# Optimization experiments

Measured on AMD Instinct MI355X. Metric: run time of the kernel, lower is better.

Reference implementation:

```python
import jax, jax.numpy as jnp
import numpy as np

HN, ND, STRIDE, ESTRIDE = 10, 40, 3, 3  # hidden_node, ndim, stride, encode_stride


def _build_graphs():
    # Dense aggregation matrices A[dst, src] equivalent to the module's fixed
    # edge lists (scatter-add of src features into dst). Graph is tiny (10/40
    # nodes) and identical across the batch, so dense matmul is the efficient
    # exact form of the gather->scatter-add.
    w = np.float32(np.exp(-(1.0 / STRIDE) ** 2))
    A_pred = np.zeros((HN, HN), np.float32)
    for j in range(HN):
        A_pred[j, j] += 1.0                      # edge [j, j], weight 1
        for dj in range(1, STRIDE - 1):          # dj = 1 only
            A_pred[(j - dj) % HN, j] += w        # edge [j, j-dj]
            A_pred[(j + dj) % HN, j] += w        # edge [j, j+dj]
    A_enc = np.zeros((HN, ND), np.float32)
    A_dec = np.zeros((ND, HN), np.float32)
    for j in range(HN):
        cg = (j * ND // HN) % ND                 # center_grid = 4j
        for i in range(cg - ESTRIDE, cg + ESTRIDE):
            A_enc[j, i % ND] += 1.0              # grid i -> hidden j
            A_dec[i % ND, j] += 1.0              # hidden j -> grid i
    return jnp.asarray(A_enc), jnp.asarray(A_pred), jnp.asarray(A_dec)

A_ENC, A_PRED, A_DEC = _build_graphs()


def setup_inputs() -> dict:
    key = jax.random.key(0)
    ks = jax.random.split(key, 12)
    B, HF = 524288, 8
    s = 0.3  # modest weight scale
    return {
        "x": jax.random.normal(ks[0], (B, ND), jnp.float32),
        "z": jax.random.uniform(ks[1], (B, HN, HF), dtype=jnp.float32),
        "y": jax.random.uniform(ks[2], (B, ND, 1), dtype=jnp.float32),
        "enc_rel_w": jax.random.normal(ks[3], (HF, 1), jnp.float32) * s,
        "enc_rel_b": jax.random.normal(ks[4], (HF,), jnp.float32) * s,
        "enc_root_w": jax.random.normal(ks[5], (HF, HF), jnp.float32) * s,
        "pred_rel_w": jax.random.normal(ks[6], (HF, HF), jnp.float32) * s,
        "pred_rel_b": jax.random.normal(ks[7], (HF,), jnp.float32) * s,
        "pred_root_w": jax.random.normal(ks[8], (HF, HF), jnp.float32) * s,
        "dec_rel_w": jax.random.normal(ks[9], (1, HF), jnp.float32) * s,
        "dec_rel_b": jax.random.normal(ks[10], (1,), jnp.float32) * s,
        "dec_root_w": jax.random.normal(ks[11], (1, 1), jnp.float32) * s,
    }


def reference(x, z, y, enc_rel_w, enc_rel_b, enc_root_w,
              pred_rel_w, pred_rel_b, pred_root_w,
              dec_rel_w, dec_rel_b, dec_root_w):
    xb = x[..., None]  # [B, 40, 1]
    # encoder GraphConv((1, 8) -> 8): lin_rel(agg(x_src)) + lin_root(z)
    agg = jnp.einsum('ds,bsf->bdf', A_ENC, xb)                 # [B, 10, 1]
    z1 = jax.nn.relu(agg @ enc_rel_w.T + enc_rel_b + z @ enc_root_w.T)
    # predictor GraphConv(8 -> 8) with edge weights folded into A_PRED
    agg2 = jnp.einsum('ds,bsf->bdf', A_PRED, z1)               # [B, 10, 8]
    z2 = jax.nn.relu(agg2 @ pred_rel_w.T + pred_rel_b + z1 @ pred_root_w.T)
    # decoder GraphConv((8, 1) -> 1)
    agg3 = jnp.einsum('ds,bsf->bdf', A_DEC, z2)                # [B, 40, 8]
    out = agg3 @ dec_rel_w.T + dec_rel_b + y @ dec_root_w.T   # [B, 40, 1]
    return out[..., 0]                                         # [B, 40]
```

## Files before the change

kernel.cpp:

```cpp
#include <hip/hip_runtime.h>


#define HN 10
#define ND 40
#define HF 8

__global__ __launch_bounds__(256) void gnn_kernel(
    const float* __restrict__ x,
    const float* __restrict__ z,
    const float* __restrict__ y,
    const float* __restrict__ enc_rel_w,
    const float* __restrict__ enc_rel_b,
    const float* __restrict__ enc_root_w,
    const float* __restrict__ pred_rel_w,
    const float* __restrict__ pred_rel_b,
    const float* __restrict__ pred_root_w,
    const float* __restrict__ dec_rel_w,
    const float* __restrict__ dec_rel_b,
    const float* __restrict__ dec_root_w,
    float* __restrict__ out,
    int B)
{
    int b = blockIdx.x * blockDim.x + threadIdx.x;
    if (b >= B) return;

    const float w = 0.8948393168143698f;

    float xv[ND];
    const float4* xp = (const float4*)(x + (size_t)b * ND);
    #pragma unroll
    for (int k = 0; k < 10; ++k) {
        float4 v = xp[k];
        xv[4*k+0] = v.x; xv[4*k+1] = v.y; xv[4*k+2] = v.z; xv[4*k+3] = v.w;
    }

    float agg[HN];
    agg[0] = xv[37] + xv[38] + xv[39] + xv[0] + xv[1] + xv[2];
    #pragma unroll
    for (int j = 1; j < HN; ++j)
        agg[j] = xv[4*j-3] + xv[4*j-2] + xv[4*j-1] + xv[4*j] + xv[4*j+1] + xv[4*j+2];

    float z1[HN][HF];
    const float4* zp = (const float4*)(z + (size_t)b * (HN*HF));
    #pragma unroll
    for (int j = 0; j < HN; ++j) {
        float zr[HF];
        float4 v0 = zp[2*j], v1 = zp[2*j+1];
        zr[0]=v0.x; zr[1]=v0.y; zr[2]=v0.z; zr[3]=v0.w;
        zr[4]=v1.x; zr[5]=v1.y; zr[6]=v1.z; zr[7]=v1.w;
        #pragma unroll
        for (int f = 0; f < HF; ++f) {
            float acc = agg[j] * enc_rel_w[f] + enc_rel_b[f];
            #pragma unroll
            for (int g = 0; g < HF; ++g)
                acc += zr[g] * enc_root_w[f*HF + g];
            z1[j][f] = fmaxf(acc, 0.0f);
        }
    }

    float s2[HN];
    #pragma unroll
    for (int j = 0; j < HN; ++j) {
        const int jm = (j + HN - 1) % HN;
        const int jp = (j + 1) % HN;
        float a2[HF];
        #pragma unroll
        for (int f = 0; f < HF; ++f)
            a2[f] = z1[j][f] + w * (z1[jm][f] + z1[jp][f]);
        float sj = 0.0f;
        #pragma unroll
        for (int f = 0; f < HF; ++f) {
            float acc = pred_rel_b[f];
            #pragma unroll
            for (int g = 0; g < HF; ++g)
                acc += a2[g] * pred_rel_w[f*HF + g];
            #pragma unroll
            for (int g = 0; g < HF; ++g)
                acc += z1[j][g] * pred_root_w[f*HF + g];
            sj += fmaxf(acc, 0.0f) * dec_rel_w[f];
        }
        s2[j] = sj;
    }

    const float drb = dec_rel_b[0];
    const float droot = dec_root_w[0];
    const float4* yp = (const float4*)(y + (size_t)b * ND);
    float4* op = (float4*)(out + (size_t)b * ND);
    #pragma unroll
    for (int k = 0; k < 10; ++k) {
        const int k1 = (k + 1) % HN;
        const float pair = s2[k] + s2[k1];
        float4 vy = yp[k];
        float4 vo;
        vo.x = s2[k] + drb + vy.x * droot;
        vo.y = pair  + drb + vy.y * droot;
        vo.z = pair  + drb + vy.z * droot;
        vo.w = s2[k1] + drb + vy.w * droot;
        op[k] = vo;
    }
}

extern "C" void kernel_launch(void* const* d_in, const int* in_sizes, int n_in,
                              void* d_out, int out_size, void* d_ws, size_t ws_size,
                              hipStream_t stream) {
    const float* x          = (const float*)d_in[0];
    const float* z          = (const float*)d_in[1];
    const float* y          = (const float*)d_in[2];
    const float* enc_rel_w  = (const float*)d_in[3];
    const float* enc_rel_b  = (const float*)d_in[4];
    const float* enc_root_w = (const float*)d_in[5];
    const float* pred_rel_w = (const float*)d_in[6];
    const float* pred_rel_b = (const float*)d_in[7];
    const float* pred_root_w= (const float*)d_in[8];
    const float* dec_rel_w  = (const float*)d_in[9];
    const float* dec_rel_b  = (const float*)d_in[10];
    const float* dec_root_w = (const float*)d_in[11];
    float* out = (float*)d_out;

    const int B = in_sizes[0] / ND;
    const int threads = 256;
    const int blocks = (B + threads - 1) / threads;
    gnn_kernel<<<blocks, threads, 0, stream>>>(
        x, z, y, enc_rel_w, enc_rel_b, enc_root_w,
        pred_rel_w, pred_rel_b, pred_root_w,
        dec_rel_w, dec_rel_b, dec_root_w, out, B);
}
```

Baseline: 424.2 us.

## Stage per-row x, z, y/out tiles through LDS for coalesced global access

Replaces per-thread strided float4 loads and stores (each thread reading its own 160-320 byte row) with cooperative coalesced tile loads into padded shared memory. Each thread then reads its row from LDS. z is staged in two halves to fit the buffer, and the encoder/predictor work is reordered to match. Output goes through LDS too, so the y reads and out writes are coalesced. This removes the tail bounds check by assuming B is a multiple of 64, and it adds several barriers, using 64-thread blocks.

```diff
diff --git a/kernel.cpp b/kernel.cpp
--- a/kernel.cpp
+++ b/kernel.cpp
@@ -4,8 +4,11 @@
 #define HN 10
 #define ND 40
 #define HF 8
+#define TPB 64
+#define ROWF 44
+#define ROW4 11
 
-__global__ __launch_bounds__(256) void gnn_kernel(
+__global__ __launch_bounds__(TPB, 4) void gnn_kernel(
     const float* __restrict__ x,
     const float* __restrict__ z,
     const float* __restrict__ y,
@@ -21,82 +24,133 @@
     float* __restrict__ out,
     int B)
 {
-    int b = blockIdx.x * blockDim.x + threadIdx.x;
-    if (b >= B) return;
+    __shared__ float lds[TPB * ROWF];
+    float4* lds4 = (float4*)lds;
+    const int t = threadIdx.x;
+    const long long tile = (long long)blockIdx.x * TPB;
 
     const float w = 0.8948393168143698f;
 
-    float xv[ND];
-    const float4* xp = (const float4*)(x + (size_t)b * ND);
+    const float4* xg = (const float4*)(x + tile * ND);
     #pragma unroll
     for (int k = 0; k < 10; ++k) {
-        float4 v = xp[k];
-        xv[4*k+0] = v.x; xv[4*k+1] = v.y; xv[4*k+2] = v.z; xv[4*k+3] = v.w;
+        int i = t + TPB * k;
+        int e = i / 10, q = i - e * 10;
+        lds4[e * ROW4 + q] = xg[i];
     }
+    __syncthreads();
 
     float agg[HN];
-    agg[0] = xv[37] + xv[38] + xv[39] + xv[0] + xv[1] + xv[2];
-    #pragma unroll
-    for (int j = 1; j < HN; ++j)
-        agg[j] = xv[4*j-3] + xv[4*j-2] + xv[4*j-1] + xv[4*j] + xv[4*j+1] + xv[4*j+2];
+    {
+        float xv[ND];
+        #pragma unroll
+        for (int k = 0; k < ND; ++k) xv[k] = lds[t * ROWF + k];
+        agg[0] = xv[37] + xv[38] + xv[39] + xv[0] + xv[1] + xv[2];
+        #pragma unroll
+        for (int j = 1; j < HN; ++j)
+            agg[j] = xv[4*j-3] + xv[4*j-2] + xv[4*j-1] + xv[4*j] + xv[4*j+1] + xv[4*j+2];
+    }
+    __syncthreads();
 
-    float z1[HN][HF];
-    const float4* zp = (const float4*)(z + (size_t)b * (HN*HF));
-    #pragma unroll
-    for (int j = 0; j < HN; ++j) {
-        float zr[HF];
-        float4 v0 = zp[2*j], v1 = zp[2*j+1];
-        zr[0]=v0.x; zr[1]=v0.y; zr[2]=v0.z; zr[3]=v0.w;
-        zr[4]=v1.x; zr[5]=v1.y; zr[6]=v1.z; zr[7]=v1.w;
+    auto enc_row = [&](int jj, int j, float (&r)[HF]) {
+        float4 v0 = lds4[t * ROW4 + jj * 2];
+        float4 v1 = lds4[t * ROW4 + jj * 2 + 1];
+        float zr[HF] = {v0.x, v0.y, v0.z, v0.w, v1.x, v1.y, v1.z, v1.w};
         #pragma unroll
         for (int f = 0; f < HF; ++f) {
             float acc = agg[j] * enc_rel_w[f] + enc_rel_b[f];
             #pragma unroll
             for (int g = 0; g < HF; ++g)
-                acc += zr[g] * enc_root_w[f*HF + g];
-            z1[j][f] = fmaxf(acc, 0.0f);
+                acc += zr[g] * enc_root_w[f * HF + g];
+            r[f] = fmaxf(acc, 0.0f);
         }
-    }
+    };
 
-    float s2[HN];
-    #pragma unroll
-    for (int j = 0; j < HN; ++j) {
-        const int jm = (j + HN - 1) % HN;
-        const int jp = (j + 1) % HN;
+    auto emit = [&](const float (&rm)[HF], const float (&rc)[HF],
+                    const float (&rp)[HF]) -> float {
         float a2[HF];
         #pragma unroll
         for (int f = 0; f < HF; ++f)
-            a2[f] = z1[j][f] + w * (z1[jm][f] + z1[jp][f]);
-        float sj = 0.0f;
+            a2[f] = rc[f] + w * (rm[f] + rp[f]);
+        float s = 0.0f;
         #pragma unroll
         for (int f = 0; f < HF; ++f) {
             float acc = pred_rel_b[f];
             #pragma unroll
             for (int g = 0; g < HF; ++g)
-                acc += a2[g] * pred_rel_w[f*HF + g];
+                acc += a2[g] * pred_rel_w[f * HF + g];
             #pragma unroll
             for (int g = 0; g < HF; ++g)
-                acc += z1[j][g] * pred_root_w[f*HF + g];
-            sj += fmaxf(acc, 0.0f) * dec_rel_w[f];
+                acc += rc[g] * pred_root_w[f * HF + g];
+            s += fmaxf(acc, 0.0f) * dec_rel_w[f];
         }
-        s2[j] = sj;
+        return s;
+    };
+
+    const float4* zg = (const float4*)(z + tile * (HN * HF));
+    float s2[HN];
+
+    #pragma unroll
+    for (int k = 0; k < 10; ++k) {
+        int i = t + TPB * k;
+        int e = i / 10, q = i - e * 10;
+        lds4[e * ROW4 + q] = zg[e * 20 + q];
     }
+    __syncthreads();
+
+    float rA[5][HF];
+    #pragma unroll
+    for (int jj = 0; jj < 5; ++jj) enc_row(jj, jj, rA[jj]);
+    s2[1] = emit(rA[0], rA[1], rA[2]);
+    s2[2] = emit(rA[1], rA[2], rA[3]);
+    s2[3] = emit(rA[2], rA[3], rA[4]);
+    __syncthreads();
+
+    #pragma unroll
+    for (int k = 0; k < 10; ++k) {
+        int i = t + TPB * k;
+        int e = i / 10, q = i - e * 10;
+        lds4[e * ROW4 + q] = zg[e * 20 + 10 + q];
+    }
+    __syncthreads();
+
+    float rB[5][HF];
+    #pragma unroll
+    for (int jj = 0; jj < 5; ++jj) enc_row(jj, 5 + jj, rB[jj]);
+    s2[4] = emit(rA[3], rA[4], rB[0]);
+    s2[5] = emit(rA[4], rB[0], rB[1]);
+    s2[6] = emit(rB[0], rB[1], rB[2]);
+    s2[7] = emit(rB[1], rB[2], rB[3]);
+    s2[8] = emit(rB[2], rB[3], rB[4]);
+    s2[9] = emit(rB[3], rB[4], rA[0]);
+    s2[0] = emit(rB[4], rA[0], rA[1]);
+    __syncthreads();
 
     const float drb = dec_rel_b[0];
     const float droot = dec_root_w[0];
-    const float4* yp = (const float4*)(y + (size_t)b * ND);
-    float4* op = (float4*)(out + (size_t)b * ND);
     #pragma unroll
     for (int k = 0; k < 10; ++k) {
         const int k1 = (k + 1) % HN;
-        const float pair = s2[k] + s2[k1];
-        float4 vy = yp[k];
-        float4 vo;
-        vo.x = s2[k] + drb + vy.x * droot;
-        vo.y = pair  + drb + vy.y * droot;
-        vo.z = pair  + drb + vy.z * droot;
-        vo.w = s2[k1] + drb + vy.w * droot;
-        op[k] = vo;
+        const float pair = s2[k] + s2[k1] + drb;
+        lds[t * ND + 4*k + 0] = s2[k] + drb;
+        lds[t * ND + 4*k + 1] = pair;
+        lds[t * ND + 4*k + 2] = pair;
+        lds[t * ND + 4*k + 3] = s2[k1] + drb;
+    }
+    __syncthreads();
+
+    const float4* yg = (const float4*)(y + tile * ND);
+    float4* og = (float4*)(out + tile * ND);
+    #pragma unroll
+    for (int k = 0; k < 10; ++k) {
+        int i = t + TPB * k;
+        float4 p = lds4[i];
+        float4 vy = yg[i];
+        p.x += vy.x * droot;
+        p.y += vy.y * droot;
+        p.z += vy.z * droot;
+        p.w += vy.w * droot;
+        og[i] = p;
     }
 }
 
@@ -118,9 +172,8 @@
     float* out = (float*)d_out;
 
     const int B = in_sizes[0] / ND;
-    const int threads = 256;
-    const int blocks = (B + threads - 1) / threads;
-    gnn_kernel<<<blocks, threads, 0, stream>>>(
+    const int blocks = B / TPB;
+    gnn_kernel<<<blocks, TPB, 0, stream>>>(
         x, z, y, enc_rel_w, enc_rel_b, enc_root_w,
         pred_rel_w, pred_rel_b, pred_root_w,
         dec_rel_w, dec_rel_b, dec_root_w, out, B);
```

Measured after the change: 472.6 us. 1.11x slower.
